# Kernel tuning notes

Measured on AMD Instinct MI355X. Metric: run time of the kernel, lower is better.

The kernel has to match this reference:

```python
import jax, jax.numpy as jnp
import numpy as np

B, S, D = 4, 2048, 512


def _dyt(x, alpha, w, b):
    return jnp.tanh(alpha * x) * w + b


def _fourier_fourier_attn(x, qr, qi, kr, ki, vr, vi, rtr, rti):
    xc = x.astype(jnp.complex64)
    qw, kw, vw, rtw = qr + 1j * qi, kr + 1j * ki, vr + 1j * vi, rtr + 1j * rti
    Xf = jnp.fft.fft(xc, axis=-1)  # [B,S,D] complex
    q = jnp.fft.fft(Xf * qw, axis=-2)
    k = jnp.fft.fft(Xf * kw, axis=-2)
    v = jnp.fft.fft(Xf * vw, axis=-2)
    rt = q / (k + 1e-12) * v
    rt = jnp.fft.ifft(rt, axis=-2) * rtw
    return jnp.fft.ifft(rt, axis=-1).real


def _fourier_sdpa(x, qr, qi, kr, ki, vr, vi):
    xc = x.astype(jnp.complex64)
    Xf = jnp.fft.fft(xc, axis=-1)
    proj = lambda w: jnp.fft.ifft(Xf * w, axis=-1).real
    q = proj(qr + 1j * qi)
    k = proj(kr + 1j * ki)
    v = proj(vr + 1j * vi)
    scores = jnp.einsum('bsd,btd->bst', q, k) / np.sqrt(D).astype(np.float32)
    attn = jax.nn.softmax(scores, axis=-1)
    return jnp.einsum('bst,btd->bsd', attn, v)


def _fourier_ffn(x, ar, ai, br, bi, bias):
    # Faithful to the source: the gelu branch is overwritten (dead code),
    # the returned value only uses the b-weighted FFT path.
    xc = x.astype(jnp.complex64)
    Xf = jnp.fft.fft(xc, axis=-1)
    h = jnp.fft.ifft(Xf * (ar + 1j * ai), axis=-1).real + bias
    h = jax.nn.gelu(h, approximate=False)  # discarded, as in the original
    return jnp.fft.ifft(Xf * (br + 1j * bi), axis=-1).real


def setup_inputs() -> dict:
    key = jax.random.key(0)
    ks = jax.random.split(key, 32)
    d = {'x': jax.random.normal(ks[0], (B, S, D), dtype=jnp.float32)}
    names_real = ['a_qr', 'a_kr', 'a_vr', 'a_rtr', 'b_qr', 'b_kr', 'b_vr', 'f_ar', 'f_br']
    names_imag = ['a_qi', 'a_ki', 'a_vi', 'a_rti', 'b_qi', 'b_ki', 'b_vi', 'f_ai', 'f_bi']
    i = 1
    for n in names_real:
        d[n] = 1.0 + 0.02 * jax.random.normal(ks[i], (D,), dtype=jnp.float32); i += 1
    for n in names_imag:
        d[n] = 0.02 * jax.random.normal(ks[i], (D,), dtype=jnp.float32); i += 1
    d['f_bias'] = 0.02 * jax.random.normal(ks[i], (D,), dtype=jnp.float32); i += 1
    for p in ['dyta', 'dytb', 'dytf']:
        d[p + '_alpha'] = jnp.full((1,), 0.5, dtype=jnp.float32)
        d[p + '_w'] = 1.0 + 0.02 * jax.random.normal(ks[i], (D,), dtype=jnp.float32); i += 1
        d[p + '_b'] = 0.02 * jax.random.normal(ks[i], (D,), dtype=jnp.float32); i += 1
    return d


def reference(x, a_qr, a_qi, a_kr, a_ki, a_vr, a_vi, a_rtr, a_rti,
              dyta_alpha, dyta_w, dyta_b,
              b_qr, b_qi, b_kr, b_ki, b_vr, b_vi,
              dytb_alpha, dytb_w, dytb_b,
              f_ar, f_ai, f_br, f_bi, f_bias,
              dytf_alpha, dytf_w, dytf_b):
    # attn_a block: FourierFourierAttention(DyT(x)) + x
    x = _fourier_fourier_attn(_dyt(x, dyta_alpha, dyta_w, dyta_b),
                              a_qr, a_qi, a_kr, a_ki, a_vr, a_vi, a_rtr, a_rti) + x
    # attn_b block: FourierScaledDotProductAttention(DyT(x)) + x
    x = _fourier_sdpa(_dyt(x, dytb_alpha, dytb_w, dytb_b),
                      b_qr, b_qi, b_kr, b_ki, b_vr, b_vi) + x
    # ffn block: FourierForwardNetwork(DyT(x)) + x
    x = _fourier_ffn(_dyt(x, dytf_alpha, dytf_w, dytf_b),
                     f_ar, f_ai, f_br, f_bi, f_bias) + x
    return x
```

## Files before the change

### kernel.cpp

```cpp
#include <hip/hip_runtime.h>


typedef __attribute__((ext_vector_type(8))) __bf16 bf16x8;
typedef __attribute__((ext_vector_type(4))) float floatx4;
typedef __attribute__((ext_vector_type(8))) _Float16 halfx8;
typedef __attribute__((ext_vector_type(8))) unsigned short ushortx8;
typedef __attribute__((ext_vector_type(2))) _Float16 half2v;
typedef __attribute__((ext_vector_type(4))) _Float16 half4v;

__device__ __forceinline__ unsigned short f2bf(float x) {
    unsigned u = __float_as_uint(x);
    u = (u + 0x7fffu + ((u >> 16) & 1u)) >> 16;
    return (unsigned short)u;
}

__device__ __forceinline__ float dyt_tanh(float x) {
    float e = __expf(2.0f * x);
    return 1.0f - 2.0f / (e + 1.0f);
}

__device__ __forceinline__ void async_load16(const unsigned short* g, unsigned short* l) {
    __builtin_amdgcn_global_load_lds(
        (const __attribute__((address_space(1))) unsigned int*)g,
        (__attribute__((address_space(3))) unsigned int*)l, 16, 0, 0);
}

__device__ __forceinline__ void wtw512(float (&tc)[12], float (&ts)[12], int lane) {
    const float w = -6.28318530717958647692f / 512.0f;
#pragma unroll
    for (int j = 0; j < 4; j++) __sincosf(w * (float)(j * 64 + lane), &ts[j], &tc[j]);
#pragma unroll
    for (int j = 0; j < 2; j++) __sincosf(w * (float)(2 * (j * 64 + lane)), &ts[4 + j], &tc[4 + j]);
    __sincosf(w * (float)(4 * lane), &ts[6], &tc[6]);
    __sincosf(w * (float)(8 * (lane & 31)), &ts[7], &tc[7]);
    __sincosf(w * (float)(16 * (lane & 15)), &ts[8], &tc[8]);
    __sincosf(w * (float)(32 * (lane & 7)), &ts[9], &tc[9]);
    __sincosf(w * (float)(64 * (lane & 3)), &ts[10], &tc[10]);
    __sincosf(w * (float)(128 * (lane & 1)), &ts[11], &tc[11]);
}

template <bool INV>
__device__ __forceinline__ void wfft512(float (&re)[8], float (&im)[8],
                                        const float (&tc)[12], const float (&ts)[12], int lane) {
    if (!INV) {
#pragma unroll
        for (int j = 0; j < 4; j++) {
            float ur = re[j], ui = im[j], vr = re[j + 4], vi = im[j + 4];
            re[j] = ur + vr; im[j] = ui + vi;
            float dr = ur - vr, di = ui - vi;
            re[j + 4] = dr * tc[j] - di * ts[j];
            im[j + 4] = dr * ts[j] + di * tc[j];
        }
#pragma unroll
        for (int g = 0; g < 8; g += 4)
#pragma unroll
            for (int jj = 0; jj < 2; jj++) {
                int j = g + jj;
                float ur = re[j], ui = im[j], vr = re[j + 2], vi = im[j + 2];
                re[j] = ur + vr; im[j] = ui + vi;
                float dr = ur - vr, di = ui - vi;
                re[j + 2] = dr * tc[4 + jj] - di * ts[4 + jj];
                im[j + 2] = dr * ts[4 + jj] + di * tc[4 + jj];
            }
#pragma unroll
        for (int j = 0; j < 8; j += 2) {
            float ur = re[j], ui = im[j], vr = re[j + 1], vi = im[j + 1];
            re[j] = ur + vr; im[j] = ui + vi;
            float dr = ur - vr, di = ui - vi;
            re[j + 1] = dr * tc[6] - di * ts[6];
            im[j + 1] = dr * ts[6] + di * tc[6];
        }
#pragma unroll
        for (int st = 0; st < 6; st++) {
            int h = 32 >> st;
            bool hi = (lane & h) != 0;
            float c = (st < 5) ? tc[7 + st] : 1.0f;
            float s = (st < 5) ? ts[7 + st] : 0.0f;
#pragma unroll
            for (int j = 0; j < 8; j++) {
                float orr = __shfl_xor(re[j], h, 64);
                float oii = __shfl_xor(im[j], h, 64);
                float dr = orr - re[j], di = oii - im[j];
                float sr = re[j] + orr, si = im[j] + oii;
                re[j] = hi ? (dr * c - di * s) : sr;
                im[j] = hi ? (dr * s + di * c) : si;
            }
        }
    } else {
#pragma unroll
        for (int st = 5; st >= 0; st--) {
            int h = 32 >> st;
            bool hi = (lane & h) != 0;
            float c = (st < 5) ? tc[7 + st] : 1.0f;
            float s = (st < 5) ? ts[7 + st] : 0.0f;
#pragma unroll
            for (int j = 0; j < 8; j++) {
                float zr = re[j], zi = im[j];
                float vr = zr * c + zi * s;
                float vi = zi * c - zr * s;
                float mr = hi ? vr : zr;
                float mi = hi ? vi : zi;
                float orr = __shfl_xor(mr, h, 64);
                float oii = __shfl_xor(mi, h, 64);
                re[j] = hi ? (orr - vr) : (zr + orr);
                im[j] = hi ? (oii - vi) : (zi + oii);
            }
        }
#pragma unroll
        for (int j = 0; j < 8; j += 2) {
            float vr = re[j + 1] * tc[6] + im[j + 1] * ts[6];
            float vi = im[j + 1] * tc[6] - re[j + 1] * ts[6];
            re[j + 1] = re[j] - vr; im[j + 1] = im[j] - vi;
            re[j] += vr; im[j] += vi;
        }
#pragma unroll
        for (int g = 0; g < 8; g += 4)
#pragma unroll
            for (int jj = 0; jj < 2; jj++) {
                int j = g + jj;
                float vr = re[j + 2] * tc[4 + jj] + im[j + 2] * ts[4 + jj];
                float vi = im[j + 2] * tc[4 + jj] - re[j + 2] * ts[4 + jj];
                re[j + 2] = re[j] - vr; im[j + 2] = im[j] - vi;
                re[j] += vr; im[j] += vi;
            }
#pragma unroll
        for (int j = 0; j < 4; j++) {
            float vr = re[j + 4] * tc[j] + im[j + 4] * ts[j];
            float vi = im[j + 4] * tc[j] - re[j + 4] * ts[j];
            re[j + 4] = re[j] - vr; im[j + 4] = im[j] - vi;
            re[j] += vr; im[j] += vi;
        }
    }
}

__global__ __launch_bounds__(256) void k1_dyt_fftd(
        const float* __restrict__ x,
        const float* __restrict__ alpha, const float* __restrict__ w, const float* __restrict__ bia,
        half2v* __restrict__ xf) {
    int tid = threadIdx.x, lane = tid & 63, wv = tid >> 6;
    size_t row = (size_t)blockIdx.x * 4 + wv;
    float tc[12], ts[12];
    wtw512(tc, ts, lane);
    float re[8], im[8];
    float a = alpha[0];
    const float* xr = x + row * 512;
#pragma unroll
    for (int j = 0; j < 8; j++) {
        int d = j * 64 + lane;
        re[j] = dyt_tanh(a * xr[d]) * w[d] + bia[d];
        im[j] = 0.f;
    }
    wfft512<false>(re, im, tc, ts, lane);
#pragma unroll
    for (int j = 0; j < 8; j++) {
        int d = j * 64 + lane;
        xf[row * 512 + d] = (half2v){(_Float16)re[j], (_Float16)im[j]};
    }
}

__device__ __forceinline__ int pidx4(int i) { return i + (i >> 3); }

__device__ __forceinline__ void r4_fwd(float4* X, int t, int h, const half2v* tw) {
    int pos = t & (h - 1);
    int i = ((t & ~(h - 1)) << 2) | pos;
    int i0 = pidx4(i), i1 = pidx4(i + h), i2 = pidx4(i + 2 * h), i3 = pidx4(i + 3 * h);
    float4 a0 = X[i0], a1 = X[i1], a2 = X[i2], a3 = X[i3];
    half2v wv = tw[pos];
    float c1 = (float)wv.x, s1 = (float)wv.y;
    float c2 = c1 * c1 - s1 * s1, s2 = 2.f * c1 * s1;
    float c3 = c2 * c1 - s2 * s1, s3 = s2 * c1 + c2 * s1;
    float4 o0, o1, o2, o3;
    {
        float t0r = a0.x + a2.x, t0i = a0.y + a2.y, t1r = a0.x - a2.x, t1i = a0.y - a2.y;
        float t2r = a1.x + a3.x, t2i = a1.y + a3.y, t3r = a1.x - a3.x, t3i = a1.y - a3.y;
        o0.x = t0r + t2r; o0.y = t0i + t2i;
        float b1r = t1r + t3i, b1i = t1i - t3r;
        float b2r = t0r - t2r, b2i = t0i - t2i;
        float b3r = t1r - t3i, b3i = t1i + t3r;
        o1.x = b1r * c1 - b1i * s1; o1.y = b1r * s1 + b1i * c1;
        o2.x = b2r * c2 - b2i * s2; o2.y = b2r * s2 + b2i * c2;
        o3.x = b3r * c3 - b3i * s3; o3.y = b3r * s3 + b3i * c3;
    }
    {
        float t0r = a0.z + a2.z, t0i = a0.w + a2.w, t1r = a0.z - a2.z, t1i = a0.w - a2.w;
        float t2r = a1.z + a3.z, t2i = a1.w + a3.w, t3r = a1.z - a3.z, t3i = a1.w - a3.w;
        o0.z = t0r + t2r; o0.w = t0i + t2i;
        float b1r = t1r + t3i, b1i = t1i - t3r;
        float b2r = t0r - t2r, b2i = t0i - t2i;
        float b3r = t1r - t3i, b3i = t1i + t3r;
        o1.z = b1r * c1 - b1i * s1; o1.w = b1r * s1 + b1i * c1;
        o2.z = b2r * c2 - b2i * s2; o2.w = b2r * s2 + b2i * c2;
        o3.z = b3r * c3 - b3i * s3; o3.w = b3r * s3 + b3i * c3;
    }
    X[i0] = o0; X[i1] = o1; X[i2] = o2; X[i3] = o3;
}

__device__ __forceinline__ void r4_inv(float4* X, int t, int h, const half2v* tw) {
    int pos = t & (h - 1);
    int i = ((t & ~(h - 1)) << 2) | pos;
    int i0 = pidx4(i), i1 = pidx4(i + h), i2 = pidx4(i + 2 * h), i3 = pidx4(i + 3 * h);
    float4 y0 = X[i0], y1 = X[i1], y2 = X[i2], y3 = X[i3];
    half2v wv = tw[pos];
    float c1 = (float)wv.x, s1 = (float)wv.y;
    float c2 = c1 * c1 - s1 * s1, s2 = 2.f * c1 * s1;
    float c3 = c2 * c1 - s2 * s1, s3 = s2 * c1 + c2 * s1;
    float4 o0, o1, o2, o3;
    {
        float u1r = y1.x * c1 + y1.y * s1, u1i = y1.y * c1 - y1.x * s1;
        float u2r = y2.x * c2 + y2.y * s2, u2i = y2.y * c2 - y2.x * s2;
        float u3r = y3.x * c3 + y3.y * s3, u3i = y3.y * c3 - y3.x * s3;
        float s0r = y0.x + u2r, s0i = y0.y + u2i;
        float s1r = y0.x - u2r, s1i = y0.y - u2i;
        float s2r = u1r + u3r, s2i = u1i + u3i;
        float s3r = u1r - u3r, s3i = u1i - u3i;
        o0.x = s0r + s2r; o0.y = s0i + s2i;
        o2.x = s0r - s2r; o2.y = s0i - s2i;
        o1.x = s1r - s3i; o1.y = s1i + s3r;
        o3.x = s1r + s3i; o3.y = s1i - s3r;
    }
    {
        float u1r = y1.z * c1 + y1.w * s1, u1i = y1.w * c1 - y1.z * s1;
        float u2r = y2.z * c2 + y2.w * s2, u2i = y2.w * c2 - y2.z * s2;
        float u3r = y3.z * c3 + y3.w * s3, u3i = y3.w * c3 - y3.z * s3;
        float s0r = y0.z + u2r, s0i = y0.w + u2i;
        float s1r = y0.z - u2r, s1i = y0.w - u2i;
        float s2r = u1r + u3r, s2i = u1i + u3i;
        float s3r = u1r - u3r, s3i = u1i - u3i;
        o0.z = s0r + s2r; o0.w = s0i + s2i;
        o2.z = s0r - s2r; o2.w = s0i - s2i;
        o1.z = s1r - s3i; o1.w = s1i + s3r;
        o3.z = s1r + s3i; o3.w = s1i - s3r;
    }
    X[i0] = o0; X[i1] = o1; X[i2] = o2; X[i3] = o3;
}

__global__ __launch_bounds__(512) void k2_sfft(
        half2v* __restrict__ xf,
        const float* __restrict__ qr, const float* __restrict__ qi,
        const float* __restrict__ kr, const float* __restrict__ ki,
        const float* __restrict__ vr, const float* __restrict__ vi,
        const float* __restrict__ rtr, const float* __restrict__ rti) {
    __shared__ float4 buf[2304];
    __shared__ half2v twd[682];
    int t = threadIdx.x;
    int g = blockIdx.x;
    int xcd = g & 7, r = g >> 3;
    int pp = xcd * 32 + (r & 31);
    int b = r >> 3 >> 2;
    b = r >> 5;
    int p0 = pp * 2;
    half4v* colh = (half4v*)(xf + (size_t)b * 2048 * 512 + p0);

    for (int i = t; i < 682; i += 512) {
        int h, off;
        if (i < 512)      { h = 512; off = 0; }
        else if (i < 640) { h = 128; off = 512; }
        else if (i < 672) { h = 32;  off = 640; }
        else if (i < 680) { h = 8;   off = 672; }
        else              { h = 2;   off = 680; }
        int pos = i - off;
        float s, c;
        __sincosf(-6.28318530717958647692f * (float)pos / (float)(4 * h), &s, &c);
        twd[i] = (half2v){(_Float16)c, (_Float16)s};
    }

#pragma unroll
    for (int c = 0; c < 4; c++) {
        int s = t + 512 * c;
        half4v h = colh[(size_t)s * 256];
        buf[pidx4(s)] = make_float4((float)h.x, (float)h.y, (float)h.z, (float)h.w);
    }
    __syncthreads(); r4_fwd(buf, t, 512, twd);
    __syncthreads(); r4_fwd(buf, t, 128, twd + 512);
    __syncthreads(); r4_fwd(buf, t, 32, twd + 640);
    __syncthreads(); r4_fwd(buf, t, 8, twd + 672);
    __syncthreads(); r4_fwd(buf, t, 2, twd + 680);
    __syncthreads();
#pragma unroll
    for (int c = 0; c < 2; c++) {
        int pr = t + 512 * c;
        int ia = pidx4(2 * pr), ib = pidx4(2 * pr + 1);
        float4 a = buf[ia], bb = buf[ib];
        buf[ia] = make_float4(a.x + bb.x, a.y + bb.y, a.z + bb.z, a.w + bb.w);
        buf[ib] = make_float4(a.x - bb.x, a.y - bb.y, a.z - bb.z, a.w - bb.w);
    }
    __syncthreads();

    int f0 = __brev((unsigned)p0) >> 23;
    int f1 = __brev((unsigned)(p0 + 1)) >> 23;
    float qw0r = qr[f0], qw0i = qi[f0], kw0r = kr[f0], kw0i = ki[f0], vw0r = vr[f0], vw0i = vi[f0];
    float qw1r = qr[f1], qw1i = qi[f1], kw1r = kr[f1], kw1i = ki[f1], vw1r = vr[f1], vw1i = vi[f1];
#pragma unroll
    for (int c = 0; c < 4; c++) {
        int idx = pidx4(t + 512 * c);
        float4 y = buf[idx];
        {
            float yr = y.x, yi = y.y;
            float qre = yr * qw0r - yi * qw0i, qim = yr * qw0i + yi * qw0r;
            float kre = yr * kw0r - yi * kw0i + 1e-12f, kim = yr * kw0i + yi * kw0r;
            float vre = yr * vw0r - yi * vw0i, vim = yr * vw0i + yi * vw0r;
            float inv = 1.0f / (kre * kre + kim * kim);
            float dre = (qre * kre + qim * kim) * inv;
            float dim = (qim * kre - qre * kim) * inv;
            y.x = dre * vre - dim * vim;
            y.y = dre * vim + dim * vre;
        }
        {
            float yr = y.z, yi = y.w;
            float qre = yr * qw1r - yi * qw1i, qim = yr * qw1i + yi * qw1r;
            float kre = yr * kw1r - yi * kw1i + 1e-12f, kim = yr * kw1i + yi * kw1r;
            float vre = yr * vw1r - yi * vw1i, vim = yr * vw1i + yi * vw1r;
            float inv = 1.0f / (kre * kre + kim * kim);
            float dre = (qre * kre + qim * kim) * inv;
            float dim = (qim * kre - qre * kim) * inv;
            y.z = dre * vre - dim * vim;
            y.w = dre * vim + dim * vre;
        }
        buf[idx] = y;
    }

    __syncthreads();
#pragma unroll
    for (int c = 0; c < 2; c++) {
        int pr = t + 512 * c;
        int ia = pidx4(2 * pr), ib = pidx4(2 * pr + 1);
        float4 a = buf[ia], bb = buf[ib];
        buf[ia] = make_float4(a.x + bb.x, a.y + bb.y, a.z + bb.z, a.w + bb.w);
        buf[ib] = make_float4(a.x - bb.x, a.y - bb.y, a.z - bb.z, a.w - bb.w);
    }
    __syncthreads(); r4_inv(buf, t, 2, twd + 680);
    __syncthreads(); r4_inv(buf, t, 8, twd + 672);
    __syncthreads(); r4_inv(buf, t, 32, twd + 640);
    __syncthreads(); r4_inv(buf, t, 128, twd + 512);
    __syncthreads(); r4_inv(buf, t, 512, twd);
    __syncthreads();

    const float sc = 1.0f / 2048.0f;
    float r0r = rtr[f0] * sc, r0i = rti[f0] * sc;
    float r1r = rtr[f1] * sc, r1i = rti[f1] * sc;
#pragma unroll
    for (int c = 0; c < 4; c++) {
        int s = t + 512 * c;
        float4 z = buf[pidx4(s)];
        float ox = z.x * r0r - z.y * r0i, oy = z.x * r0i + z.y * r0r;
        float oz = z.z * r1r - z.w * r1i, ow = z.z * r1i + z.w * r1r;
        colh[(size_t)s * 256] = (half4v){(_Float16)ox, (_Float16)oy, (_Float16)oz, (_Float16)ow};
    }
}

__global__ __launch_bounds__(256) void k3_mid(
        const half2v* __restrict__ xf,
        const float* __restrict__ x,
        const float* __restrict__ alpha, const float* __restrict__ w, const float* __restrict__ bia,
        const float* __restrict__ qr, const float* __restrict__ qi,
        const float* __restrict__ kr, const float* __restrict__ ki,
        const float* __restrict__ vr, const float* __restrict__ vi,
        float* __restrict__ x1,
        unsigned short* __restrict__ qb, unsigned short* __restrict__ kb, unsigned short* __restrict__ vb) {
    __shared__ __align__(16) char smem[4 * 1024 * 8];
    int tid = threadIdx.x, lane = tid & 63, wv = tid >> 6;
    float2* zb = (float2*)(smem + wv * 8192);
    float* wbs = (float*)smem;
    float2* zf = (float2*)(smem + 12288 + wv * 4096);
    size_t pr = (size_t)blockIdx.x * 4 + wv;
    size_t r1 = pr * 2, r2 = r1 + 1;
    float tc[12], ts[12];
    wtw512(tc, ts, lane);

    float xa[8], xb2[8];
#pragma unroll
    for (int j = 0; j < 8; j++) {
        int d = j * 64 + lane;
        half2v h1 = xf[r1 * 512 + d];
        half2v h2 = xf[r2 * 512 + d];
        zb[d]       = make_float2((float)h1.x, (float)h1.y);
        zb[512 + d] = make_float2((float)h2.x, (float)h2.y);
        xa[j]  = x[r1 * 512 + d];
        xb2[j] = x[r2 * 512 + d];
    }
    float re[8], im[8];
#pragma unroll
    for (int j = 0; j < 8; j++) {
        int d = j * 64 + lane;
        int fd = __brev((unsigned)d) >> 23;
        int dp = __brev((unsigned)((512 - fd) & 511)) >> 23;
        float2 z1 = zb[d], z1p = zb[dp];
        float2 z2 = zb[512 + d], z2p = zb[512 + dp];
        float h1r = 0.5f * (z1.x + z1p.x), h1i = 0.5f * (z1.y - z1p.y);
        float h2r = 0.5f * (z2.x + z2p.x), h2i = 0.5f * (z2.y - z2p.y);
        re[j] = h1r - h2i;
        im[j] = h1i + h2r;
    }
    __syncthreads();
    for (int idx = tid; idx < 512; idx += 256) {
        int f = __brev((unsigned)idx) >> 23;
        int gg = (512 - f) & 511;
        float aa = (f == 0 || f == 256) ? 0.04419417382415922f : 0.0625f;
        float ah = aa * 0.5f;
        const float s5 = 0.5f * (1.0f / 512.0f);
        wbs[0 * 512 + idx] = ah * (qr[f] + qr[gg]); wbs[1 * 512 + idx] = ah * (qi[f] - qi[gg]);
        wbs[2 * 512 + idx] = ah * (kr[f] + kr[gg]); wbs[3 * 512 + idx] = ah * (ki[f] - ki[gg]);
        wbs[4 * 512 + idx] = s5 * (vr[f] + vr[gg]); wbs[5 * 512 + idx] = s5 * (vi[f] - vi[gg]);
    }

    wfft512<true>(re, im, tc, ts, lane);
    float a = alpha[0];
    float gre[8], gim[8];
#pragma unroll
    for (int j = 0; j < 8; j++) {
        int d = j * 64 + lane;
        float v1 = re[j] * (1.0f / 512.0f) + xa[j];
        float v2 = im[j] * (1.0f / 512.0f) + xb2[j];
        x1[r1 * 512 + d] = v1;
        x1[r2 * 512 + d] = v2;
        gre[j] = dyt_tanh(a * v1) * w[d] + bia[d];
        gim[j] = dyt_tanh(a * v2) * w[d] + bia[d];
    }
    wfft512<false>(gre, gim, tc, ts, lane);
    __syncthreads();

#pragma unroll
    for (int j = 0; j < 8; j++)
        zf[j * 64 + lane] = make_float2(gre[j], gim[j]);

    float pvr[8], pvi[8];
#pragma unroll
    for (int j = 0; j < 8; j++) {
        int i = j * 64 + lane;
        float wr0 = wbs[4 * 512 + i], wi0 = wbs[5 * 512 + i];
        pvr[j] = gre[j] * wr0 - gim[j] * wi0;
        pvi[j] = gre[j] * wi0 + gim[j] * wr0;
    }

    bool odd = (lane & 1) != 0;
#pragma unroll
    for (int j = 0; j < 8; j++) {
        int d = j * 64 + lane;
        int fd = __brev((unsigned)d) >> 23;
        int dp = __brev((unsigned)((512 - fd) & 511)) >> 23;
        float2 Zp = zf[dp];
        float zr = gre[j], zi = gim[j];
        float A1r = 0.5f * (zr + Zp.x), A1i = 0.5f * (zi - Zp.y);
        float A2r = 0.5f * (zi + Zp.y), A2i = 0.5f * (Zp.x - zr);
        float wr0 = wbs[0 * 512 + d], wi0 = wbs[1 * 512 + d];
        float Q1r = A1r * wr0 - A1i * wi0, Q1i = A1r * wi0 + A1i * wr0;
        float Q2r = A2r * wr0 - A2i * wi0, Q2i = A2r * wi0 + A2i * wr0;
        qb[r1 * 512 + d] = f2bf(odd ? -Q1i : Q1r);
        qb[r2 * 512 + d] = f2bf(odd ? -Q2i : Q2r);
        float wr1 = wbs[2 * 512 + d], wi1 = wbs[3 * 512 + d];
        float K1r = A1r * wr1 - A1i * wi1, K1i = A1r * wi1 + A1i * wr1;
        float K2r = A2r * wr1 - A2i * wi1, K2i = A2r * wi1 + A2i * wr1;
        kb[r1 * 512 + d] = f2bf(odd ? -K1i : K1r);
        kb[r2 * 512 + d] = f2bf(odd ? -K2i : K2r);
    }

    wfft512<true>(pvr, pvi, tc, ts, lane);
#pragma unroll
    for (int j = 0; j < 8; j++) {
        int d = j * 64 + lane;
        vb[r1 * 512 + d] = f2bf(pvr[j]);
        vb[r2 * 512 + d] = f2bf(pvi[j]);
    }
}

__global__ __launch_bounds__(256) void gemm_bt(
        const unsigned short* __restrict__ A, const unsigned short* __restrict__ Bt,
        void* __restrict__ C, int M, int N, int Ks, int kseg, float scale, int out_half) {
    int tilesM = M >> 7, tilesN = N >> 7;
    int perBatch = tilesM * tilesN;
    int l = blockIdx.x;
    int seg = blockIdx.y;
    int s = l & 7, t = l >> 3;
    int cnt = perBatch >> 3;
    int bz = t / cnt;
    int u = t - bz * cnt;
    int pn = tilesN >> 1, pm = tilesM >> 2;
    int n0 = ((s & 1) * pn + (u % pn)) << 7;
    int m0 = ((s >> 1) * pm + (u / pn)) << 7;
    int kbase = seg * kseg;

    const unsigned short* Ab = A + (size_t)bz * M * Ks;
    const unsigned short* Bb = Bt + (size_t)bz * N * Ks;
    __shared__ __align__(16) unsigned short smem[2 * 128 * 64];
    unsigned short* As = smem;
    unsigned short* Bs = smem + 128 * 64;
    int tid = threadIdx.x;
    int wave = tid >> 6, lane = tid & 63;
    int wm = (wave >> 1) * 64, wn = (wave & 1) * 64;
    int lrow = lane & 15, lq = lane >> 4;
    floatx4 acc[4][4];
#pragma unroll
    for (int i = 0; i < 4; i++)
#pragma unroll
        for (int j = 0; j < 4; j++)
            acc[i][j] = (floatx4){0.f, 0.f, 0.f, 0.f};

    int lr = lane >> 3;
    int lcs = lane & 7;
    for (int k0 = kbase; k0 < kbase + kseg; k0 += 64) {
        __syncthreads();
#pragma unroll
        for (int i = 0; i < 4; i++) {
            int c = wave * 4 + i;
            int r = c * 8 + lr;
            int gcol = ((lcs ^ (r & 7)) << 3);
            async_load16(Ab + (size_t)(m0 + r) * Ks + k0 + gcol, As + c * 512);
            async_load16(Bb + (size_t)(n0 + r) * Ks + k0 + gcol, Bs + c * 512);
        }
        __syncthreads();
        bf16x8 a0[4], a1[4], b0[4], b1[4];
#pragma unroll
        for (int mi = 0; mi < 4; mi++) {
            int r = wm + mi * 16 + lrow;
            a0[mi] = *(const bf16x8*)(As + r * 64 + ((lq ^ (r & 7)) << 3));
            a1[mi] = *(const bf16x8*)(As + r * 64 + (((lq + 4) ^ (r & 7)) << 3));
        }
#pragma unroll
        for (int ni = 0; ni < 4; ni++) {
            int r = wn + ni * 16 + lrow;
            b0[ni] = *(const bf16x8*)(Bs + r * 64 + ((lq ^ (r & 7)) << 3));
            b1[ni] = *(const bf16x8*)(Bs + r * 64 + (((lq + 4) ^ (r & 7)) << 3));
        }
#pragma unroll
        for (int mi = 0; mi < 4; mi++)
#pragma unroll
            for (int ni = 0; ni < 4; ni++) {
                acc[mi][ni] = __builtin_amdgcn_mfma_f32_16x16x32_bf16(a0[mi], b0[ni], acc[mi][ni], 0, 0, 0);
                acc[mi][ni] = __builtin_amdgcn_mfma_f32_16x16x32_bf16(a1[mi], b1[ni], acc[mi][ni], 0, 0, 0);
            }
    }
    size_t cbase = ((size_t)seg * 4 + bz) * (size_t)M * N;
    int lr0 = (wave >> 1) * 16 + lq * 4;
    for (int mi = 0; mi < 4; mi++) {
        __syncthreads();
        if (out_half) {
            _Float16* Cs = (_Float16*)smem;
            for (int ni = 0; ni < 4; ni++)
                for (int r = 0; r < 4; r++)
                    Cs[(lr0 + r) * 128 + wn + ni * 16 + lrow] = (_Float16)(acc[mi][ni][r] * scale);
            __syncthreads();
            for (int h = 0; h < 2; h++) {
                int chunk = tid + h * 256;
                int rl = chunk >> 4, cb = (chunk & 15) * 16;
                int grow = m0 + mi * 16 + (rl & 15) + (rl >> 4) * 64;
                *(uint4*)((char*)C + (cbase + (size_t)grow * N + n0) * 2 + cb) =
                    *(const uint4*)((const char*)Cs + rl * 256 + cb);
            }
        } else {
            float* Cs = (float*)smem;
            for (int ni = 0; ni < 4; ni++)
                for (int r = 0; r < 4; r++)
                    Cs[(lr0 + r) * 128 + wn + ni * 16 + lrow] = acc[mi][ni][r] * scale;
            __syncthreads();
            for (int h = 0; h < 4; h++) {
                int chunk = tid + h * 256;
                int rl = chunk >> 5, cb = (chunk & 31) * 16;
                int grow = m0 + mi * 16 + (rl & 15) + (rl >> 4) * 64;
                *(uint4*)((char*)C + (cbase + (size_t)grow * N + n0) * 4 + cb) =
                    *(const uint4*)((const char*)Cs + rl * 512 + cb);
            }
        }
    }
}

__global__ __launch_bounds__(256) void sm_tr(
        const _Float16* __restrict__ Sc, unsigned short* __restrict__ P,
        const unsigned short* __restrict__ vb, unsigned short* __restrict__ vT) {
    __shared__ __align__(16) char lds[64 * 65 * 2];
    if (blockIdx.x < 8192) {
        float* red = (float*)lds;
        int tid = threadIdx.x;
        size_t row = blockIdx.x;
        halfx8 hv = *(const halfx8*)(Sc + row * 2048 + tid * 8);
        float v[8];
#pragma unroll
        for (int j = 0; j < 8; j++) v[j] = (float)hv[j];
        float mx = v[0];
#pragma unroll
        for (int j = 1; j < 8; j++) mx = fmaxf(mx, v[j]);
        for (int off = 32; off >= 1; off >>= 1) mx = fmaxf(mx, __shfl_xor(mx, off));
        int wv = tid >> 6;
        if ((tid & 63) == 0) red[wv] = mx;
        __syncthreads();
        mx = fmaxf(fmaxf(red[0], red[1]), fmaxf(red[2], red[3]));
        float e[8], sum = 0.f;
#pragma unroll
        for (int j = 0; j < 8; j++) { e[j] = __expf(v[j] - mx); sum += e[j]; }
        for (int off = 32; off >= 1; off >>= 1) sum += __shfl_xor(sum, off);
        __syncthreads();
        if ((tid & 63) == 0) red[wv] = sum;
        __syncthreads();
        float inv = 1.0f / (red[0] + red[1] + red[2] + red[3]);
        ushortx8 o;
#pragma unroll
        for (int j = 0; j < 8; j++) o[j] = f2bf(e[j] * inv);
        *(ushortx8*)(P + row * 2048 + tid * 8) = o;
    } else {
        unsigned short (*tile)[65] = (unsigned short (*)[65])lds;
        int id = blockIdx.x - 8192;
        int sx = id & 31, dy = (id >> 5) & 7, bz = id >> 8;
        int s0 = sx * 64, d0 = dy * 64;
        int tx = threadIdx.x & 63, ty = threadIdx.x >> 6;
        for (int j = 0; j < 16; j++) {
            int s = ty + j * 4;
            tile[s][tx] = vb[((size_t)bz * 2048 + s0 + s) * 512 + d0 + tx];
        }
        __syncthreads();
        for (int j = 0; j < 16; j++) {
            int d = ty + j * 4;
            vT[((size_t)bz * 512 + d0 + d) * 2048 + s0 + tx] = tile[tx][d];
        }
    }
}

__global__ __launch_bounds__(256) void k5_ffn(
        const float* __restrict__ attn0, const float* __restrict__ attn1,
        const float* __restrict__ x1,
        const float* __restrict__ alpha, const float* __restrict__ w, const float* __restrict__ bia,
        const float* __restrict__ br, const float* __restrict__ bi,
        float* __restrict__ out) {
    __shared__ float wbs[2][512];
    int tid = threadIdx.x, lane = tid & 63, wv = tid >> 6;
    size_t pr = (size_t)blockIdx.x * 4 + wv;
    size_t r1 = pr * 2, r2 = r1 + 1;
    for (int idx = tid; idx < 512; idx += 256) {
        int f = __brev((unsigned)idx) >> 23;
        int gg = (512 - f) & 511;
        wbs[0][idx] = 0.5f * (br[f] + br[gg]) * (1.0f / 512.0f);
        wbs[1][idx] = 0.5f * (bi[f] - bi[gg]) * (1.0f / 512.0f);
    }
    float tc[12], ts[12];
    wtw512(tc, ts, lane);
    float a = alpha[0];
    float re[8], im[8], x2a[8], x2b[8];
#pragma unroll
    for (int j = 0; j < 8; j++) {
        int d = j * 64 + lane;
        float v1 = attn0[r1 * 512 + d] + attn1[r1 * 512 + d] + x1[r1 * 512 + d];
        float v2 = attn0[r2 * 512 + d] + attn1[r2 * 512 + d] + x1[r2 * 512 + d];
        x2a[j] = v1; x2b[j] = v2;
        re[j] = dyt_tanh(a * v1) * w[d] + bia[d];
        im[j] = dyt_tanh(a * v2) * w[d] + bia[d];
    }
    wfft512<false>(re, im, tc, ts, lane);
    __syncthreads();
#pragma unroll
    for (int j = 0; j < 8; j++) {
        int i = j * 64 + lane;
        float wr0 = wbs[0][i], wi0 = wbs[1][i];
        float rr = re[j], ii = im[j];
        re[j] = rr * wr0 - ii * wi0;
        im[j] = rr * wi0 + ii * wr0;
    }
    wfft512<true>(re, im, tc, ts, lane);
#pragma unroll
    for (int j = 0; j < 8; j++) {
        int d = j * 64 + lane;
        out[r1 * 512 + d] = re[j] + x2a[j];
        out[r2 * 512 + d] = im[j] + x2b[j];
    }
}

extern "C" void kernel_launch(void* const* d_in, const int* in_sizes, int n_in,
                              void* d_out, int out_size, void* d_ws, size_t ws_size,
                              hipStream_t stream) {
    const float* x      = (const float*)d_in[0];
    const float* a_qr   = (const float*)d_in[1];
    const float* a_kr   = (const float*)d_in[2];
    const float* a_vr   = (const float*)d_in[3];
    const float* a_rtr  = (const float*)d_in[4];
    const float* b_qr   = (const float*)d_in[5];
    const float* b_kr   = (const float*)d_in[6];
    const float* b_vr   = (const float*)d_in[7];
    const float* f_br   = (const float*)d_in[9];
    const float* a_qi   = (const float*)d_in[10];
    const float* a_ki   = (const float*)d_in[11];
    const float* a_vi   = (const float*)d_in[12];
    const float* a_rti  = (const float*)d_in[13];
    const float* b_qi   = (const float*)d_in[14];
    const float* b_ki   = (const float*)d_in[15];
    const float* b_vi   = (const float*)d_in[16];
    const float* f_bi   = (const float*)d_in[18];
    const float* dyta_alpha = (const float*)d_in[20];
    const float* dyta_w     = (const float*)d_in[21];
    const float* dyta_b     = (const float*)d_in[22];
    const float* dytb_alpha = (const float*)d_in[23];
    const float* dytb_w     = (const float*)d_in[24];
    const float* dytb_b     = (const float*)d_in[25];
    const float* dytf_alpha = (const float*)d_in[26];
    const float* dytf_w     = (const float*)d_in[27];
    const float* dytf_b     = (const float*)d_in[28];
    (void)in_sizes; (void)n_in; (void)out_size; (void)ws_size;

    char* ws = (char*)d_ws;
    const size_t MB = 1024 * 1024;
    half2v* xfH = (half2v*)(ws + 0 * MB);
    float* x1   = (float*)(ws + 32 * MB);
    unsigned short* qb = (unsigned short*)(ws + 48 * MB);
    unsigned short* kb = (unsigned short*)(ws + 56 * MB);
    unsigned short* vb = (unsigned short*)(ws + 64 * MB);
    unsigned short* vT = (unsigned short*)(ws + 72 * MB);
    _Float16* scores   = (_Float16*)(ws + 0 * MB);
    unsigned short* Pb = (unsigned short*)(ws + 0 * MB);
    float* attnP       = (float*)(ws + 81 * MB);
    float* outp = (float*)d_out;

    k1_dyt_fftd<<<2048, 256, 0, stream>>>(x, dyta_alpha, dyta_w, dyta_b, xfH);
    k2_sfft<<<1024, 512, 0, stream>>>(xfH, a_qr, a_qi, a_kr, a_ki, a_vr, a_vi, a_rtr, a_rti);
    k3_mid<<<1024, 256, 0, stream>>>(xfH, x, dytb_alpha, dytb_w, dytb_b,
                                     b_qr, b_qi, b_kr, b_ki, b_vr, b_vi, x1, qb, kb, vb);
    gemm_bt<<<1024, 256, 0, stream>>>(qb, kb, scores, 2048, 2048, 512, 512,
                                      0.04419417382415922f, 1);
    sm_tr<<<9216, 256, 0, stream>>>(scores, Pb, vb, vT);
    gemm_bt<<<dim3(256, 2), 256, 0, stream>>>(Pb, vT, attnP, 2048, 512, 2048, 1024,
                                              1.0f, 0);
    k5_ffn<<<1024, 256, 0, stream>>>(attnP, attnP + (size_t)4 * 2048 * 512, x1,
                                     dytf_alpha, dytf_w, dytf_b, f_br, f_bi, outp);
}
```

Measured before the change: 284.2 us.

## Double-buffer GEMM LDS tiles and store split-K partials as fp16

The bf16 GEMM kernel now keeps two LDS stages and issues the async global-to-LDS loads for the next K tile while computing the current one, with one barrier per iteration instead of two. This hides load latency behind MFMA work, at the cost of doubling shared memory to 64 KB per block, which may lower occupancy. The split-K partial outputs of the P·V GEMM are now written as fp16 instead of fp32 and read back as fp16 in the FFN kernel, halving that intermediate traffic at some precision cost. A redundant index computation is also cleaned up.

Result: no change. 286.8 us (+0.9%).

```diff
diff --git a/kernel.cpp b/kernel.cpp
--- a/kernel.cpp
+++ b/kernel.cpp
@@ -246,8 +246,7 @@
     int g = blockIdx.x;
     int xcd = g & 7, r = g >> 3;
     int pp = xcd * 32 + (r & 31);
-    int b = r >> 3 >> 2;
-    b = r >> 5;
+    int b = r >> 5;
     int p0 = pp * 2;
     half4v* colh = (half4v*)(xf + (size_t)b * 2048 * 512 + p0);
 
@@ -478,16 +477,17 @@
     int n0 = ((s & 1) * pn + (u % pn)) << 7;
     int m0 = ((s >> 1) * pm + (u / pn)) << 7;
     int kbase = seg * kseg;
+    int kend = kbase + kseg;
 
     const unsigned short* Ab = A + (size_t)bz * M * Ks;
     const unsigned short* Bb = Bt + (size_t)bz * N * Ks;
-    __shared__ __align__(16) unsigned short smem[2 * 128 * 64];
-    unsigned short* As = smem;
-    unsigned short* Bs = smem + 128 * 64;
+    __shared__ __align__(16) unsigned short smem[4 * 128 * 64];
     int tid = threadIdx.x;
     int wave = tid >> 6, lane = tid & 63;
     int wm = (wave >> 1) * 64, wn = (wave & 1) * 64;
     int lrow = lane & 15, lq = lane >> 4;
+    int lr = lane >> 3;
+    int lcs = lane & 7;
     floatx4 acc[4][4];
 #pragma unroll
     for (int i = 0; i < 4; i++)
@@ -495,19 +495,26 @@
         for (int j = 0; j < 4; j++)
             acc[i][j] = (floatx4){0.f, 0.f, 0.f, 0.f};
 
-    int lr = lane >> 3;
-    int lcs = lane & 7;
-    for (int k0 = kbase; k0 < kbase + kseg; k0 += 64) {
-        __syncthreads();
+    auto STAGE = [&](int kk, int bufi) {
+        unsigned short* Asb = smem + bufi * 16384;
+        unsigned short* Bsb = Asb + 8192;
 #pragma unroll
         for (int i = 0; i < 4; i++) {
             int c = wave * 4 + i;
             int r = c * 8 + lr;
             int gcol = ((lcs ^ (r & 7)) << 3);
-            async_load16(Ab + (size_t)(m0 + r) * Ks + k0 + gcol, As + c * 512);
-            async_load16(Bb + (size_t)(n0 + r) * Ks + k0 + gcol, Bs + c * 512);
-        }
-        __syncthreads();
+            async_load16(Ab + (size_t)(m0 + r) * Ks + kk + gcol, Asb + c * 512);
+            async_load16(Bb + (size_t)(n0 + r) * Ks + kk + gcol, Bsb + c * 512);
+        }
+    };
+
+    STAGE(kbase, 0);
+    __syncthreads();
+    int cur = 0;
+    for (int k0 = kbase; k0 < kend; k0 += 64) {
+        if (k0 + 64 < kend) STAGE(k0 + 64, cur ^ 1);
+        const unsigned short* As = smem + cur * 16384;
+        const unsigned short* Bs = As + 8192;
         bf16x8 a0[4], a1[4], b0[4], b1[4];
 #pragma unroll
         for (int mi = 0; mi < 4; mi++) {
@@ -528,6 +535,8 @@
                 acc[mi][ni] = __builtin_amdgcn_mfma_f32_16x16x32_bf16(a0[mi], b0[ni], acc[mi][ni], 0, 0, 0);
                 acc[mi][ni] = __builtin_amdgcn_mfma_f32_16x16x32_bf16(a1[mi], b1[ni], acc[mi][ni], 0, 0, 0);
             }
+        __syncthreads();
+        cur ^= 1;
     }
     size_t cbase = ((size_t)seg * 4 + bz) * (size_t)M * N;
     int lr0 = (wave >> 1) * 16 + lq * 4;
@@ -614,7 +623,7 @@
 }
 
 __global__ __launch_bounds__(256) void k5_ffn(
-        const float* __restrict__ attn0, const float* __restrict__ attn1,
+        const _Float16* __restrict__ attn0, const _Float16* __restrict__ attn1,
         const float* __restrict__ x1,
         const float* __restrict__ alpha, const float* __restrict__ w, const float* __restrict__ bia,
         const float* __restrict__ br, const float* __restrict__ bi,
@@ -636,8 +645,8 @@
 #pragma unroll
     for (int j = 0; j < 8; j++) {
         int d = j * 64 + lane;
-        float v1 = attn0[r1 * 512 + d] + attn1[r1 * 512 + d] + x1[r1 * 512 + d];
-        float v2 = attn0[r2 * 512 + d] + attn1[r2 * 512 + d] + x1[r2 * 512 + d];
+        float v1 = (float)attn0[r1 * 512 + d] + (float)attn1[r1 * 512 + d] + x1[r1 * 512 + d];
+        float v2 = (float)attn0[r2 * 512 + d] + (float)attn1[r2 * 512 + d] + x1[r2 * 512 + d];
         x2a[j] = v1; x2b[j] = v2;
         re[j] = dyt_tanh(a * v1) * w[d] + bia[d];
         im[j] = dyt_tanh(a * v2) * w[d] + bia[d];
@@ -702,7 +711,7 @@
     unsigned short* vT = (unsigned short*)(ws + 72 * MB);
     _Float16* scores   = (_Float16*)(ws + 0 * MB);
     unsigned short* Pb = (unsigned short*)(ws + 0 * MB);
-    float* attnP       = (float*)(ws + 81 * MB);
+    _Float16* attnP    = (_Float16*)(ws + 81 * MB);
     float* outp = (float*)d_out;
 
     k1_dyt_fftd<<<2048, 256, 0, stream>>>(x, dyta_alpha, dyta_w, dyta_b, xfH);
@@ -713,7 +722,7 @@
                                       0.04419417382415922f, 1);
     sm_tr<<<9216, 256, 0, stream>>>(scores, Pb, vb, vT);
     gemm_bt<<<dim3(256, 2), 256, 0, stream>>>(Pb, vT, attnP, 2048, 512, 2048, 1024,
-                                              1.0f, 0);
+                                              1.0f, 1);
     k5_ffn<<<1024, 256, 0, stream>>>(attnP, attnP + (size_t)4 * 2048 * 512, x1,
                                      dytf_alpha, dytf_w, dytf_b, f_br, f_bi, outp);
 }
```
